# Performance work log

Measured on AMD Instinct MI355X. Metric: run time of the kernel, lower is better.

Reference implementation:

```python
import jax, jax.numpy as jnp
import numpy as np

VOCAB = 100000
PAD_ID = VOCAB - 2
INTEREST_ID = VOCAB - 1


def setup_inputs() -> dict:
    key = jax.random.key(0)
    k1, k2, k3 = jax.random.split(key, 3)
    B, S, H = 1024, 200, 128
    hidden_states = jax.random.normal(k1, (B, S, H), dtype=jnp.float32)
    input_ids = jax.random.randint(k2, (B, S), 0, VOCAB, dtype=jnp.int64)
    w_proj = jax.random.normal(k3, (H,), dtype=jnp.float32) * (1.0 / np.sqrt(H))
    b_proj = jnp.zeros((1,), dtype=jnp.float32)
    return {"hidden_states": hidden_states, "input_ids": input_ids,
            "w_proj": w_proj, "b_proj": b_proj}


def reference(hidden_states, input_ids, w_proj, b_proj):
    # hidden_states: [B, S, H]; input_ids: [B, S]
    B, S, H = hidden_states.shape
    mask = (input_ids != PAD_ID) & (input_ids != INTEREST_ID)  # [B, S]
    # additive attention: queries = hidden, keys = first token state
    keys = hidden_states[:, 0:1, :]                 # [B, 1, H]
    features = jnp.tanh(hidden_states + keys)       # [B, S, H]
    scores = jnp.einsum('bsh,h->bs', features, w_proj) + b_proj[0]
    scores = jnp.where(mask, scores, -jnp.inf)
    attention_weights = jax.nn.softmax(scores, axis=-1)  # [B, S]
    # scatter-add attention weights into vocab-sized output (duplicate ids accumulate)
    batch_idx = jnp.arange(B)[:, None]              # [B, 1]
    repeat_probs = jnp.zeros((B, VOCAB), dtype=hidden_states.dtype)
    repeat_probs = repeat_probs.at[batch_idx, input_ids].add(attention_weights)
    return repeat_probs
```

## Files before the change

### kernel.cpp

```cpp
#include <hip/hip_runtime.h>
#include <math.h>

#define B_           1024
#define S_           200
#define H_           128
#define VOCAB_       100000
#define PAD_ID_      99998
#define INTEREST_ID_ 99999
#define NTHREADS_    512

typedef float vfloat4 __attribute__((ext_vector_type(4)));

__global__ __launch_bounds__(NTHREADS_) void rd90220_fused_v5(
    const float* __restrict__ hs,
    const int*   __restrict__ ids,
    const float* __restrict__ w,
    const float* __restrict__ bp,
    float*       __restrict__ out)
{
    __shared__ float s_scores[S_];
    __shared__ float s_red[16];

    const int batch = blockIdx.x;
    const int tid   = threadIdx.x;
    const int wave  = tid >> 6;
    const int lane  = tid & 63;
    const int half  = lane >> 5;
    const int hl    = lane & 31;

    const float* hsb  = hs + (size_t)batch * (S_ * H_);
    float*       rowo = out + (size_t)batch * VOCAB_;

    {
        vfloat4* rowo4 = (vfloat4*)rowo;
        const vfloat4 z = {0.f, 0.f, 0.f, 0.f};
        #pragma unroll 4
        for (int i = tid; i < VOCAB_ / 4; i += NTHREADS_)
            __builtin_nontemporal_store(z, rowo4 + i);
    }

    int   id    = 0;
    bool  valid = false;
    if (tid < S_) {
        id    = ids[batch * S_ + tid];
        valid = (id != PAD_ID_) && (id != INTEREST_ID_);
    }

    const vfloat4 key = ((const vfloat4*)hsb)[hl];
    const vfloat4 wv  = ((const vfloat4*)w)[hl];

    for (int s0 = wave * 2; s0 < S_; s0 += 16) {
        const int s = s0 + half;
        const vfloat4 x =
            __builtin_nontemporal_load(((const vfloat4*)(hsb + s * H_)) + hl);
        float acc = tanhf(x.x + key.x) * wv.x
                  + tanhf(x.y + key.y) * wv.y
                  + tanhf(x.z + key.z) * wv.z
                  + tanhf(x.w + key.w) * wv.w;
        #pragma unroll
        for (int off = 16; off; off >>= 1)
            acc += __shfl_xor(acc, off, 64);
        if (hl == 0) s_scores[s] = acc;
    }

    __syncthreads();

    const float bias = bp[0];
    float sc = (tid < S_ && valid) ? (s_scores[tid] + bias) : -INFINITY;

    float m = sc;
    #pragma unroll
    for (int off = 32; off; off >>= 1)
        m = fmaxf(m, __shfl_down(m, off, 64));
    if (lane == 0) s_red[wave] = m;
    __syncthreads();
    m = fmaxf(fmaxf(fmaxf(s_red[0], s_red[1]), fmaxf(s_red[2], s_red[3])),
              fmaxf(fmaxf(s_red[4], s_red[5]), fmaxf(s_red[6], s_red[7])));

    const float e = (tid < S_ && valid) ? expf(sc - m) : 0.0f;
    float t = e;
    #pragma unroll
    for (int off = 32; off; off >>= 1)
        t += __shfl_down(t, off, 64);
    if (lane == 0) s_red[8 + wave] = t;
    __syncthreads();
    const float sum = (s_red[8]  + s_red[9])  + (s_red[10] + s_red[11])
                    + (s_red[12] + s_red[13]) + (s_red[14] + s_red[15]);

    if (tid < S_ && valid) {
        atomicAdd(&rowo[id], e / sum);
    }
}

extern "C" void kernel_launch(void* const* d_in, const int* in_sizes, int n_in,
                              void* d_out, int out_size, void* d_ws, size_t ws_size,
                              hipStream_t stream) {
    const float* hs  = (const float*)d_in[0];
    const int*   ids = (const int*)d_in[1];
    const float* w   = (const float*)d_in[2];
    const float* bp  = (const float*)d_in[3];
    float*       out = (float*)d_out;

    rd90220_fused_v5<<<B_, NTHREADS_, 0, stream>>>(hs, ids, w, bp, out);
}
```

Measured before the change: 508.6 us.

## Specialize waves: half zero the output row, half compute scores with prefetch

Splits the block's eight waves into two roles. Four waves zero the vocab-sized output row while the other four compute attention scores, prefetching the next hidden-state row one step ahead in a fully unrolled loop. The aim is to overlap the store-heavy zeroing with the load- and tanh-heavy scoring instead of running them back to back in every wave. In exchange each role has half the threads, so the zero-fill and the score loop are each more serialized per wave, and the full unroll raises register pressure.

```diff
diff --git a/kernel.cpp b/kernel.cpp
--- a/kernel.cpp
+++ b/kernel.cpp
@@ -11,7 +11,7 @@
 
 typedef float vfloat4 __attribute__((ext_vector_type(4)));
 
-__global__ __launch_bounds__(NTHREADS_) void rd90220_fused_v5(
+__global__ __launch_bounds__(NTHREADS_) void rd90220_fused_v6(
     const float* __restrict__ hs,
     const int*   __restrict__ ids,
     const float* __restrict__ w,
@@ -25,18 +25,43 @@
     const int tid   = threadIdx.x;
     const int wave  = tid >> 6;
     const int lane  = tid & 63;
-    const int half  = lane >> 5;
-    const int hl    = lane & 31;
 
     const float* hsb  = hs + (size_t)batch * (S_ * H_);
     float*       rowo = out + (size_t)batch * VOCAB_;
 
-    {
+    if (wave < 4) {
         vfloat4* rowo4 = (vfloat4*)rowo;
         const vfloat4 z = {0.f, 0.f, 0.f, 0.f};
-        #pragma unroll 4
-        for (int i = tid; i < VOCAB_ / 4; i += NTHREADS_)
+        for (int i = tid; i < VOCAB_ / 4; i += 256)
             __builtin_nontemporal_store(z, rowo4 + i);
+    } else {
+        const int w4   = wave - 4;
+        const int half = lane >> 5;
+        const int hl   = lane & 31;
+
+        const vfloat4 key = ((const vfloat4*)hsb)[hl];
+        const vfloat4 wv  = ((const vfloat4*)w)[hl];
+
+        const int sbase = w4 * 2 + half;
+        vfloat4 x = __builtin_nontemporal_load(
+            ((const vfloat4*)(hsb + sbase * H_)) + hl);
+        #pragma unroll
+        for (int i = 0; i < 25; ++i) {
+            const vfloat4 cur = x;
+            if (i + 1 < 25) {
+                const int sn = (i + 1) * 8 + sbase;
+                x = __builtin_nontemporal_load(
+                    ((const vfloat4*)(hsb + sn * H_)) + hl);
+            }
+            float acc = tanhf(cur.x + key.x) * wv.x
+                      + tanhf(cur.y + key.y) * wv.y
+                      + tanhf(cur.z + key.z) * wv.z
+                      + tanhf(cur.w + key.w) * wv.w;
+            #pragma unroll
+            for (int off = 16; off; off >>= 1)
+                acc += __shfl_xor(acc, off, 64);
+            if (hl == 0) s_scores[i * 8 + sbase] = acc;
+        }
     }
 
     int   id    = 0;
@@ -44,23 +69,6 @@
     if (tid < S_) {
         id    = ids[batch * S_ + tid];
         valid = (id != PAD_ID_) && (id != INTEREST_ID_);
-    }
-
-    const vfloat4 key = ((const vfloat4*)hsb)[hl];
-    const vfloat4 wv  = ((const vfloat4*)w)[hl];
-
-    for (int s0 = wave * 2; s0 < S_; s0 += 16) {
-        const int s = s0 + half;
-        const vfloat4 x =
-            __builtin_nontemporal_load(((const vfloat4*)(hsb + s * H_)) + hl);
-        float acc = tanhf(x.x + key.x) * wv.x
-                  + tanhf(x.y + key.y) * wv.y
-                  + tanhf(x.z + key.z) * wv.z
-                  + tanhf(x.w + key.w) * wv.w;
-        #pragma unroll
-        for (int off = 16; off; off >>= 1)
-            acc += __shfl_xor(acc, off, 64);
-        if (hl == 0) s_scores[s] = acc;
     }
 
     __syncthreads();
@@ -101,5 +109,5 @@
     const float* bp  = (const float*)d_in[3];
     float*       out = (float*)d_out;
 
-    rd90220_fused_v5<<<B_, NTHREADS_, 0, stream>>>(hs, ids, w, bp, out);
+    rd90220_fused_v6<<<B_, NTHREADS_, 0, stream>>>(hs, ids, w, bp, out);
 }
```

Result: no change. 513.2 us (+0.9%).
